# Performance work log

Measured on AMD Instinct MI355X. Metric: run time of the kernel, lower is better.

Reference implementation:

```python
import jax, jax.numpy as jnp
import numpy as np
from jax import lax

# norse LIF/LI default parameters
DT = 0.001
TAU_SYN_INV = 200.0   # 1/5e-3
TAU_MEM_INV = 100.0   # 1/1e-2
V_TH = 1.0
V_LEAK = 0.0
V_RESET = 0.0
ALPHA = 100.0         # SuperSpike surrogate slope (method='super')
SEQ_LEN = 40          # LIFConstantCurrentEncoder(40)
SCALE = 50.0

@jax.custom_vjp
def heaviside(x):
    # forward: spike if x > 0; backward: SuperSpike surrogate
    return (x > 0).astype(x.dtype)

def _h_fwd(x):
    return (x > 0).astype(x.dtype), x

def _h_bwd(x, g):
    return (g / (ALPHA * jnp.abs(x) + 1.0) ** 2,)

heaviside.defvjp(_h_fwd, _h_bwd)

def constant_current_encode(current):
    # LIF membrane driven by a constant input current; emit spike train (T, B, F)
    def step(v, _):
        v = v + DT * TAU_MEM_INV * ((V_LEAK - v) + current)
        z = heaviside(v - V_TH)
        v = (1.0 - z) * v  # reset to zero on spike
        return v, z
    _, spikes = lax.scan(step, jnp.zeros_like(current), None, length=SEQ_LEN)
    return spikes

def setup_inputs() -> dict:
    key = jax.random.key(0)
    k1, k2, k3, k4 = jax.random.split(key, 4)
    batch, state_dim, hidden, out = 65536, 4, 128, 2
    x = jax.random.normal(k1, (batch, state_dim), jnp.float32)
    s_in = np.float32(np.sqrt(1.0 / (2 * state_dim)))
    s_hid = np.float32(np.sqrt(1.0 / hidden))
    w_in = jax.random.normal(k2, (hidden, 2 * state_dim), jnp.float32) * s_in   # LIFCell input weights
    w_rec = jax.random.normal(k3, (hidden, hidden), jnp.float32) * s_hid        # LIFCell recurrent weights
    w_out = jax.random.normal(k4, (out, hidden), jnp.float32) * s_hid           # LICell readout weights
    return {"x": x, "w_in": w_in, "w_rec": w_rec, "w_out": w_out}

def reference(x, w_in, w_rec, w_out):
    # encode positive / negative parts of the (scaled) observation into spikes
    x_pos = constant_current_encode(jax.nn.relu(SCALE * x))   # (T, B, 4)
    x_neg = constant_current_encode(jax.nn.relu(-SCALE * x))  # (T, B, 4)
    spikes = jnp.concatenate([x_pos, x_neg], axis=2)          # (T, B, 8)

    B = x.shape[0]
    H = w_in.shape[0]
    O = w_out.shape[0]
    z0 = jnp.zeros((B, H), x.dtype)
    v0 = jnp.zeros((B, H), x.dtype)
    i0 = jnp.zeros((B, H), x.dtype)
    vo0 = jnp.zeros((B, O), x.dtype)
    io0 = jnp.zeros((B, O), x.dtype)

    def step(carry, xt):
        z, v, i, vo, io = carry
        # --- LIFCell (recurrent spiking layer) ---
        i_dec = i - DT * TAU_SYN_INV * i
        v_dec = v + DT * TAU_MEM_INV * ((V_LEAK - v) + i)
        z_new = heaviside(v_dec - V_TH)
        v_new = (1.0 - z_new) * v_dec + z_new * V_RESET
        i_new = i_dec + xt @ w_in.T + z @ w_rec.T
        # dropout(p=0.5) is identity in eval mode
        # --- LICell (leaky-integrator readout) ---
        vo_new = vo + DT * TAU_MEM_INV * ((V_LEAK - vo) + io)
        io_new = io - DT * TAU_SYN_INV * io + z_new @ w_out.T
        return (z_new, v_new, i_new, vo_new, io_new), vo_new

    _, voltages = lax.scan(step, (z0, v0, i0, vo0, io0), spikes)  # (T, B, 2)
    m = jnp.max(voltages, axis=0)
    return jax.nn.softmax(m, axis=1)
```

## Files before the change

### kernel.cpp

```cpp
#include <hip/hip_runtime.h>


#pragma clang fp contract(off)

typedef float f32x4 __attribute__((ext_vector_type(4)));
typedef float f32x2 __attribute__((ext_vector_type(2)));
typedef short short8 __attribute__((ext_vector_type(8)));
typedef int int4v __attribute__((ext_vector_type(4)));

constexpr int TSTEPS = 40;

__device__ __forceinline__ unsigned rnbf(float f) {
    unsigned u = __float_as_uint(f);
    return (u + 0x7FFFu + ((u >> 16) & 1u)) & 0xFFFF0000u;
}

__device__ __forceinline__ void split2pair(float a, float b,
                                           unsigned& hi, unsigned& mi) {
    unsigned ha = rnbf(a), hb = rnbf(b);
    float ra = a - __uint_as_float(ha);
    float rb = b - __uint_as_float(hb);
    unsigned ma = rnbf(ra), mb = rnbf(rb);
    hi = (ha >> 16) | (hb & 0xFFFF0000u);
    mi = (ma >> 16) | (mb & 0xFFFF0000u);
}

__device__ __forceinline__ f32x4 mfma16(int4v a, int4v b, f32x4 c) {
    return __builtin_amdgcn_mfma_f32_16x16x32_bf16(
        __builtin_bit_cast(short8, a), __builtin_bit_cast(short8, b), c, 0, 0, 0);
}

template <int CTRL>
__device__ __forceinline__ float dpp_mov(float v) {
    return __int_as_float(
        __builtin_amdgcn_update_dpp(0, __float_as_int(v), CTRL, 0xF, 0xF, true));
}

__device__ __forceinline__ f32x2 lo2(f32x4 a) {
    return __builtin_shufflevector(a, a, 0, 1);
}
__device__ __forceinline__ f32x2 hi2(f32x4 a) {
    return __builtin_shufflevector(a, a, 2, 3);
}

__global__ __launch_bounds__(256, 3) void snn_kernel(
    const float* __restrict__ x,
    const float* __restrict__ w_in,
    const float* __restrict__ w_rec,
    const float* __restrict__ w_out,
    float* __restrict__ out)
{
    __shared__ __align__(16) char zraw[8192];
    __shared__ __align__(16) char axtlds[TSTEPS * 512];
    __shared__ float crlds[TSTEPS][16][2];

    const int tid = threadIdx.x;
    const int l   = tid & 63;
    const int wv  = tid >> 6;
    const int cl  = l & 15;
    const int kg  = l >> 4;
    const int kb  = kg * 8;
    const int b0  = blockIdx.x * 16;
    const int Ns  = wv * 32;
    const int des = blockIdx.x & 3;

    const f32x2 P1  = {0.1f, 0.1f};
    const f32x2 P02 = {0.2f, 0.2f};

    int4v BrecHi[2][4], BrecMi[2][4];
#pragma unroll
    for (int t = 0; t < 2; ++t) {
        int n = Ns + t * 16 + cl;
#pragma unroll
        for (int kc = 0; kc < 4; ++kc) {
            const float* wp = w_rec + n * 128 + kc * 32 + kb;
            float4 wa = *reinterpret_cast<const float4*>(wp);
            float4 wb = *reinterpret_cast<const float4*>(wp + 4);
            float w8[8] = {wa.x, wa.y, wa.z, wa.w, wb.x, wb.y, wb.z, wb.w};
#pragma unroll
            for (int r = 0; r < 4; ++r) {
                unsigned h, m;
                split2pair(w8[2 * r], w8[2 * r + 1], h, m);
                BrecHi[t][kc][r] = (int)h;
                BrecMi[t][kc][r] = (int)m;
            }
        }
    }

    int4v BwinPk[2];
#pragma unroll
    for (int t = 0; t < 2; ++t) {
        int n = Ns + t * 16 + cl;
        float w8[8];
#pragma unroll
        for (int j = 0; j < 8; ++j)
            w8[j] = (kg < 2) ? w_in[n * 8 + j] : 0.0f;
#pragma unroll
        for (int r = 0; r < 4; ++r) {
            unsigned h, m;
            split2pair(w8[2 * r], w8[2 * r + 1], h, m);
            BwinPk[t][r] = (int)(kg == 0 ? h : (kg == 1 ? m : 0u));
        }
    }

    int4v Bwout[4];
    {
        int  ch   = cl & 1;
        int  part = (cl >> 1) & 1;
        bool act  = cl < 4;
#pragma unroll
        for (int kc = 0; kc < 4; ++kc) {
            float w8[8];
#pragma unroll
            for (int j = 0; j < 8; ++j)
                w8[j] = act ? w_out[ch * 128 + kc * 32 + kb + j] : 0.0f;
#pragma unroll
            for (int r = 0; r < 4; ++r) {
                unsigned h, m;
                split2pair(w8[2 * r], w8[2 * r + 1], h, m);
                Bwout[kc][r] = (int)(part ? m : h);
            }
        }
    }

    if (wv == des) {
        float xv0 = x[(size_t)(b0 + (l >> 3)) * 4 + (l & 3)];
        float xv1 = x[(size_t)(b0 + 8 + (l >> 3)) * 4 + (l & 3)];
        float s0 = 50.0f * xv0, s1 = 50.0f * xv1;
        f32x2 cur, ve = {0.0f, 0.0f};
        cur[0] = (l & 4) ? fmaxf(-s0, 0.0f) : fmaxf(s0, 0.0f);
        cur[1] = (l & 4) ? fmaxf(-s1, 0.0f) : fmaxf(s1, 0.0f);
#pragma unroll 1
        for (int u = 0; u < TSTEPS; ++u) {
            f32x2 te = cur - ve;
            f32x2 vv = ve + P1 * te;
            bool e0 = vv[0] > 1.0f, e1 = vv[1] > 1.0f;
            unsigned long long bm0 = __ballot(e0), bm1 = __ballot(e1);
            ve[0] = e0 ? 0.0f : vv[0];
            ve[1] = e1 ? 0.0f : vv[1];
            unsigned long long src = (cl < 8) ? (bm0 >> (cl * 8))
                                              : (bm1 >> ((cl - 8) * 8));
            unsigned byt = (unsigned)src & 0xFFu;
            int4v axt;
            axt[0] = (int)(((byt & 1u)   ? 0x3F80u : 0u) | ((byt & 2u)   ? 0x3F800000u : 0u));
            axt[1] = (int)(((byt & 4u)   ? 0x3F80u : 0u) | ((byt & 8u)   ? 0x3F800000u : 0u));
            axt[2] = (int)(((byt & 16u)  ? 0x3F80u : 0u) | ((byt & 32u)  ? 0x3F800000u : 0u));
            axt[3] = (int)(((byt & 64u)  ? 0x3F80u : 0u) | ((byt & 128u) ? 0x3F800000u : 0u));
            if (l < 32)
                *reinterpret_cast<int4v*>(&axtlds[u * 512 + l * 16]) = axt;
        }
    }

    f32x2 iSl[2] = {{0,0},{0,0}}, iSh[2] = {{0,0},{0,0}};
    f32x2 vSl[2] = {{0,0},{0,0}}, vSh[2] = {{0,0},{0,0}};

    unsigned awrb[2];
#pragma unroll
    for (int t = 0; t < 2; ++t) {
        int col = Ns + t * 16 + cl;
        awrb[t] = (unsigned)((kg * 1024 + col * 2) ^ ((kg & 1) << 6));
    }
    unsigned ard = (unsigned)((cl * 256 + kg * 16) ^ ((cl & 7) << 4)) | 4096u;

    auto loadfrags = [&](int4v* zf) {
#pragma unroll
        for (int kc = 0; kc < 4; ++kc)
            zf[kc] = *reinterpret_cast<int4v*>(&zraw[ard ^ (unsigned)(kc << 6)]);
    };

    auto readout_cr = [&](const int4v* zf, int slot) {
        f32x4 cro = {0,0,0,0};
#pragma unroll
        for (int kc = 0; kc < 4; ++kc) cro = mfma16(zf[kc], Bwout[kc], cro);
        f32x4 cr;
#pragma unroll
        for (int r = 0; r < 4; ++r) cr[r] = cro[r] + dpp_mov<0x4E>(cro[r]);
        if (cl < 2) {
#pragma unroll
            for (int r = 0; r < 4; ++r) crlds[slot][kg * 4 + r][cl] = cr[r];
        }
    };

    auto encoder_lif = [&](int u, bool with_rec, const int4v* zf) {
        int4v axt = *reinterpret_cast<const int4v*>(
            &axtlds[u * 512 + (l & 31) * 16]);
#pragma unroll
        for (int t = 0; t < 2; ++t) {
            f32x4 cin = {0,0,0,0};
            cin = mfma16(axt, BwinPk[t], cin);
            f32x4 crec = {0,0,0,0};
            if (with_rec) {
#pragma unroll
                for (int kc = 0; kc < 4; ++kc)
                    crec = mfma16(zf[kc], BrecMi[t][kc], crec);
#pragma unroll
                for (int kc = 0; kc < 4; ++kc)
                    crec = mfma16(zf[kc], BrecHi[t][kc], crec);
            }
            f32x2 idl = iSl[t] - P02 * iSl[t];
            f32x2 idh = iSh[t] - P02 * iSh[t];
            f32x2 ttl = iSl[t] - vSl[t];
            f32x2 tth = iSh[t] - vSh[t];
            f32x2 vdl = vSl[t] + P1 * ttl;
            f32x2 vdh = vSh[t] + P1 * tth;
#pragma unroll
            for (int r = 0; r < 4; ++r) {
                float vdr = (r < 2) ? vdl[r] : vdh[r - 2];
                bool zb = vdr > 1.0f;
                float vres = zb ? 0.0f : vdr;
                if (r == 0)      vSl[t][0] = vres;
                else if (r == 1) vSl[t][1] = vres;
                else if (r == 2) vSh[t][0] = vres;
                else             vSh[t][1] = vres;
                short zv = zb ? (short)0x3F80 : (short)0;
                unsigned a = (awrb[t] ^ (unsigned)(r << 4)) + (unsigned)(r * 256);
                *reinterpret_cast<short*>(&zraw[a]) = zv;
            }
            iSl[t] = (idl + lo2(cin)) + lo2(crec);
            iSh[t] = (idh + hi2(cin)) + hi2(crec);
        }
    };

    auto toggle = [&]() {
        ard ^= 4096u;
        awrb[0] ^= 4096u;
        awrb[1] ^= 4096u;
    };

    __syncthreads();
    encoder_lif(0, false, nullptr);
    __syncthreads();
    toggle();

#pragma unroll 1
    for (int u = 1; u < TSTEPS; ++u) {
        int4v zf[4];
        loadfrags(zf);
        if (wv == (u & 3)) readout_cr(zf, u - 1);
        encoder_lif(u, true, zf);
        __syncthreads();
        toggle();
    }

    if (wv == des) {
        int4v zf[4];
        loadfrags(zf);
        readout_cr(zf, TSTEPS - 1);
        f32x4 io = {0,0,0,0}, vo = {0,0,0,0};
        f32x4 mx = {-3e38f,-3e38f,-3e38f,-3e38f};
        const int ch = cl & 1;
#pragma unroll 1
        for (int u = 0; u < TSTEPS; ++u) {
            f32x4 cr4;
#pragma unroll
            for (int r = 0; r < 4; ++r) cr4[r] = crlds[u][kg * 4 + r][ch];
            f32x4 vn;
#pragma unroll
            for (int r = 0; r < 4; ++r) {
                float t2 = io[r] - vo[r];
                vn[r] = vo[r] + 0.1f * t2;
            }
#pragma unroll
            for (int r = 0; r < 4; ++r)
                io[r] = (io[r] - 0.2f * io[r]) + cr4[r];
            vo = vn;
#pragma unroll
            for (int r = 0; r < 4; ++r) mx[r] = fmaxf(mx[r], vn[r]);
        }
#pragma unroll
        for (int r = 0; r < 4; ++r) {
            float partner = dpp_mov<0xB1>(mx[r]);
            float mm = fmaxf(mx[r], partner);
            float es = expf(mx[r] - mm);
            float ep = expf(partner - mm);
            float inv = 1.0f / (es + ep);
            float pr = es * inv;
            if (cl < 2) out[(size_t)(b0 + kg * 4 + r) * 2 + cl] = pr;
        }
    }
}

extern "C" void kernel_launch(void* const* d_in, const int* in_sizes, int n_in,
                              void* d_out, int out_size, void* d_ws, size_t ws_size,
                              hipStream_t stream) {
    const float* x     = (const float*)d_in[0];
    const float* w_in  = (const float*)d_in[1];
    const float* w_rec = (const float*)d_in[2];
    const float* w_out = (const float*)d_in[3];
    float* out = (float*)d_out;

    int B = in_sizes[0] / 4;
    int blocks = B / 16;
    snn_kernel<<<blocks, 256, 0, stream>>>(x, w_in, w_rec, w_out, out);
}
```

Baseline: 240.7 us.

## Precompute bf16-split weight fragments in a prep kernel and split encoder writes across waves

```diff
diff --git a/kernel.cpp b/kernel.cpp
--- a/kernel.cpp
+++ b/kernel.cpp
@@ -9,6 +9,7 @@
 typedef int int4v __attribute__((ext_vector_type(4)));
 
 constexpr int TSTEPS = 40;
+
 
 __device__ __forceinline__ unsigned rnbf(float f) {
     unsigned u = __float_as_uint(f);
@@ -43,11 +44,72 @@
     return __builtin_shufflevector(a, a, 2, 3);
 }
 
+__global__ void prep_kernel(const float* __restrict__ w_in,
+                            const float* __restrict__ w_rec,
+                            const float* __restrict__ w_out,
+                            int4v* __restrict__ ws)
+{
+    int gid = blockIdx.x * 256 + threadIdx.x;
+    if (gid < 2048) {
+        int l = gid & 63, set = gid >> 6;
+        int cl = l & 15, kg = l >> 4, kb = kg * 8;
+        int wv = set >> 3, t = (set >> 2) & 1;
+        int n = wv * 32 + t * 16 + cl;
+        int kc = set & 3;
+        const float* wp = w_rec + n * 128 + kc * 32 + kb;
+        int4v hi, mi;
+#pragma unroll
+        for (int r = 0; r < 4; ++r) {
+            unsigned h, m;
+            split2pair(wp[2 * r], wp[2 * r + 1], h, m);
+            hi[r] = (int)h;
+            mi[r] = (int)m;
+        }
+        ws[set * 64 + l] = hi;
+        ws[2048 + set * 64 + l] = mi;
+    } else if (gid < 2560) {
+        int g = gid - 2048;
+        int l = g & 63, set = g >> 6;
+        int cl = l & 15, kg = l >> 4;
+        int wv = set >> 1, t = set & 1;
+        int n = wv * 32 + t * 16 + cl;
+        float w8[8];
+#pragma unroll
+        for (int j = 0; j < 8; ++j)
+            w8[j] = (kg < 2) ? w_in[n * 8 + j] : 0.0f;
+        int4v f;
+#pragma unroll
+        for (int r = 0; r < 4; ++r) {
+            unsigned h, m;
+            split2pair(w8[2 * r], w8[2 * r + 1], h, m);
+            f[r] = (int)(kg == 0 ? h : (kg == 1 ? m : 0u));
+        }
+        ws[4096 + set * 64 + l] = f;
+    } else if (gid < 2816) {
+        int g = gid - 2560;
+        int l = g & 63, kc = g >> 6;
+        int cl = l & 15, kg = l >> 4, kb = kg * 8;
+        int  ch   = cl & 1;
+        int  part = (cl >> 1) & 1;
+        bool act  = cl < 4;
+        float w8[8];
+#pragma unroll
+        for (int j = 0; j < 8; ++j)
+            w8[j] = act ? w_out[ch * 128 + kc * 32 + kb + j] : 0.0f;
+        int4v f;
+#pragma unroll
+        for (int r = 0; r < 4; ++r) {
+            unsigned h, m;
+            split2pair(w8[2 * r], w8[2 * r + 1], h, m);
+            f[r] = (int)(part ? m : h);
+        }
+        ws[4608 + kc * 64 + l] = f;
+    }
+}
+
 __global__ __launch_bounds__(256, 3) void snn_kernel(
     const float* __restrict__ x,
-    const float* __restrict__ w_in,
-    const float* __restrict__ w_rec,
-    const float* __restrict__ w_out,
+    const int4v* __restrict__ ws,
     float* __restrict__ out)
 {
     __shared__ __align__(16) char zraw[8192];
@@ -59,7 +121,6 @@
     const int wv  = tid >> 6;
     const int cl  = l & 15;
     const int kg  = l >> 4;
-    const int kb  = kg * 8;
     const int b0  = blockIdx.x * 16;
     const int Ns  = wv * 32;
     const int des = blockIdx.x & 3;
@@ -69,67 +130,30 @@
 
     int4v BrecHi[2][4], BrecMi[2][4];
 #pragma unroll
-    for (int t = 0; t < 2; ++t) {
-        int n = Ns + t * 16 + cl;
+    for (int t = 0; t < 2; ++t)
 #pragma unroll
         for (int kc = 0; kc < 4; ++kc) {
-            const float* wp = w_rec + n * 128 + kc * 32 + kb;
-            float4 wa = *reinterpret_cast<const float4*>(wp);
-            float4 wb = *reinterpret_cast<const float4*>(wp + 4);
-            float w8[8] = {wa.x, wa.y, wa.z, wa.w, wb.x, wb.y, wb.z, wb.w};
-#pragma unroll
-            for (int r = 0; r < 4; ++r) {
-                unsigned h, m;
-                split2pair(w8[2 * r], w8[2 * r + 1], h, m);
-                BrecHi[t][kc][r] = (int)h;
-                BrecMi[t][kc][r] = (int)m;
-            }
-        }
-    }
-
+            int set = wv * 8 + t * 4 + kc;
+            BrecHi[t][kc] = ws[set * 64 + l];
+            BrecMi[t][kc] = ws[2048 + set * 64 + l];
+        }
     int4v BwinPk[2];
 #pragma unroll
-    for (int t = 0; t < 2; ++t) {
-        int n = Ns + t * 16 + cl;
-        float w8[8];
-#pragma unroll
-        for (int j = 0; j < 8; ++j)
-            w8[j] = (kg < 2) ? w_in[n * 8 + j] : 0.0f;
-#pragma unroll
-        for (int r = 0; r < 4; ++r) {
-            unsigned h, m;
-            split2pair(w8[2 * r], w8[2 * r + 1], h, m);
-            BwinPk[t][r] = (int)(kg == 0 ? h : (kg == 1 ? m : 0u));
-        }
-    }
-
+    for (int t = 0; t < 2; ++t)
+        BwinPk[t] = ws[4096 + (wv * 2 + t) * 64 + l];
     int4v Bwout[4];
+#pragma unroll
+    for (int kc = 0; kc < 4; ++kc)
+        Bwout[kc] = ws[4608 + kc * 64 + l];
+
     {
-        int  ch   = cl & 1;
-        int  part = (cl >> 1) & 1;
-        bool act  = cl < 4;
-#pragma unroll
-        for (int kc = 0; kc < 4; ++kc) {
-            float w8[8];
-#pragma unroll
-            for (int j = 0; j < 8; ++j)
-                w8[j] = act ? w_out[ch * 128 + kc * 32 + kb + j] : 0.0f;
-#pragma unroll
-            for (int r = 0; r < 4; ++r) {
-                unsigned h, m;
-                split2pair(w8[2 * r], w8[2 * r + 1], h, m);
-                Bwout[kc][r] = (int)(part ? m : h);
-            }
-        }
-    }
-
-    if (wv == des) {
         float xv0 = x[(size_t)(b0 + (l >> 3)) * 4 + (l & 3)];
         float xv1 = x[(size_t)(b0 + 8 + (l >> 3)) * 4 + (l & 3)];
         float s0 = 50.0f * xv0, s1 = 50.0f * xv1;
         f32x2 cur, ve = {0.0f, 0.0f};
         cur[0] = (l & 4) ? fmaxf(-s0, 0.0f) : fmaxf(s0, 0.0f);
         cur[1] = (l & 4) ? fmaxf(-s1, 0.0f) : fmaxf(s1, 0.0f);
+        const int ulo = wv * 10, uhi = ulo + 10;
 #pragma unroll 1
         for (int u = 0; u < TSTEPS; ++u) {
             f32x2 te = cur - ve;
@@ -138,16 +162,18 @@
             unsigned long long bm0 = __ballot(e0), bm1 = __ballot(e1);
             ve[0] = e0 ? 0.0f : vv[0];
             ve[1] = e1 ? 0.0f : vv[1];
-            unsigned long long src = (cl < 8) ? (bm0 >> (cl * 8))
-                                              : (bm1 >> ((cl - 8) * 8));
-            unsigned byt = (unsigned)src & 0xFFu;
-            int4v axt;
-            axt[0] = (int)(((byt & 1u)   ? 0x3F80u : 0u) | ((byt & 2u)   ? 0x3F800000u : 0u));
-            axt[1] = (int)(((byt & 4u)   ? 0x3F80u : 0u) | ((byt & 8u)   ? 0x3F800000u : 0u));
-            axt[2] = (int)(((byt & 16u)  ? 0x3F80u : 0u) | ((byt & 32u)  ? 0x3F800000u : 0u));
-            axt[3] = (int)(((byt & 64u)  ? 0x3F80u : 0u) | ((byt & 128u) ? 0x3F800000u : 0u));
-            if (l < 32)
-                *reinterpret_cast<int4v*>(&axtlds[u * 512 + l * 16]) = axt;
+            if (u >= ulo && u < uhi) {
+                unsigned long long src = (cl < 8) ? (bm0 >> (cl * 8))
+                                                  : (bm1 >> ((cl - 8) * 8));
+                unsigned byt = (unsigned)src & 0xFFu;
+                int4v axt;
+                axt[0] = (int)(((byt & 1u)   ? 0x3F80u : 0u) | ((byt & 2u)   ? 0x3F800000u : 0u));
+                axt[1] = (int)(((byt & 4u)   ? 0x3F80u : 0u) | ((byt & 8u)   ? 0x3F800000u : 0u));
+                axt[2] = (int)(((byt & 16u)  ? 0x3F80u : 0u) | ((byt & 32u)  ? 0x3F800000u : 0u));
+                axt[3] = (int)(((byt & 64u)  ? 0x3F80u : 0u) | ((byt & 128u) ? 0x3F800000u : 0u));
+                if (l < 32)
+                    *reinterpret_cast<int4v*>(&axtlds[u * 512 + l * 16]) = axt;
+            }
         }
     }
 
@@ -288,8 +314,11 @@
     const float* w_rec = (const float*)d_in[2];
     const float* w_out = (const float*)d_in[3];
     float* out = (float*)d_out;
+    int4v* ws = (int4v*)d_ws;
+
+    prep_kernel<<<11, 256, 0, stream>>>(w_in, w_rec, w_out, ws);
 
     int B = in_sizes[0] / 4;
     int blocks = B / 16;
-    snn_kernel<<<blocks, 256, 0, stream>>>(x, w_in, w_rec, w_out, out);
-}
+    snn_kernel<<<blocks, 256, 0, stream>>>(x, ws, out);
+}
```

Measured after the change: 220.6 us (median of 2 runs). 8.4% less time.
